# Performance work log

Hardware: AMD Instinct MI355X
Metric: run time of the kernel (lower is better)

The kernel has to match this reference:

```python
import jax, jax.numpy as jnp
import numpy as np

N, E, F, D, G, K = 50000, 1600000, 128, 256, 64, 10


def setup_inputs() -> dict:
    key = jax.random.key(0)
    ks = jax.random.split(key, 20)
    x = jax.random.normal(ks[0], (N, F), dtype=jnp.float32)
    edge_index = jax.random.randint(ks[1], (2, E), 0, N, dtype=jnp.int64)
    batch_index = jnp.sort(jax.random.randint(ks[2], (N,), 0, G, dtype=jnp.int64))

    def lin(k, fan_in, fan_out):
        w = jax.random.normal(k, (fan_in, fan_out), dtype=jnp.float32) / np.sqrt(fan_in)
        return w

    return {
        "x": x, "edge_index": edge_index, "batch_index": batch_index,
        "W0": lin(ks[3], F, D), "b0": jnp.zeros((D,), jnp.float32),
        "W1": lin(ks[4], D, D), "b1": jnp.zeros((D,), jnp.float32),
        "W2": lin(ks[5], D, D), "b2": jnp.zeros((D,), jnp.float32),
        "W3": lin(ks[6], D, D), "b3": jnp.zeros((D,), jnp.float32),
        "fc1_w": lin(ks[7], 2 * D, 512), "fc1_b": jnp.zeros((512,), jnp.float32),
        "fc2_w": lin(ks[8], 512, 256), "fc2_b": jnp.zeros((256,), jnp.float32),
        "out_w": lin(ks[9], 256, K), "out_b": jnp.zeros((K,), jnp.float32),
    }


def _gcn_conv(x, W, b, src, dst, dis):
    # PyG GCNConv: h = x W; out = D^{-1/2}(A+I)D^{-1/2} h + b  (self-loops added)
    h = x @ W                                   # [N, D]
    norm = dis[src] * dis[dst]                  # [E]
    msg = h[src] * norm[:, None]                # [E, D]
    agg = jax.ops.segment_sum(msg, dst, num_segments=x.shape[0])
    agg = agg + h * (dis * dis)[:, None]        # self-loop contribution
    return agg + b


def reference(x, edge_index, batch_index, W0, b0, W1, b1, W2, b2, W3, b3,
              fc1_w, fc1_b, fc2_w, fc2_b, out_w, out_b):
    src, dst = edge_index[0], edge_index[1]
    n = x.shape[0]
    # degree with self-loops
    deg = 1.0 + jax.ops.segment_sum(jnp.ones((src.shape[0],), jnp.float32), dst,
                                    num_segments=n)
    dis = jax.lax.rsqrt(deg)

    h = jnp.tanh(_gcn_conv(x, W0, b0, src, dst, dis))
    h = jnp.tanh(_gcn_conv(h, W1, b1, src, dst, dis))
    h = jnp.tanh(_gcn_conv(h, W2, b2, src, dst, dis))
    h = jnp.tanh(_gcn_conv(h, W3, b3, src, dst, dis))

    # global max pool + global mean pool over graphs in the batch
    gmax = jax.ops.segment_max(h, batch_index, num_segments=G)
    gsum = jax.ops.segment_sum(h, batch_index, num_segments=G)
    cnt = jax.ops.segment_sum(jnp.ones((n,), jnp.float32), batch_index,
                              num_segments=G)
    gmean = gsum / jnp.maximum(cnt, 1.0)[:, None]
    g = jnp.concatenate([gmax, gmean], axis=1)  # [G, 2D]

    g = jax.nn.relu(g @ fc1_w + fc1_b)
    g = jax.nn.relu(g @ fc2_w + fc2_b)
    return g @ out_w + out_b
```

## Files before the change

kernel.cpp:

```cpp
#include <hip/hip_runtime.h>
#include <hip/hip_bf16.h>


#define NNODES 50000
#define DDIM 256
#define SCAN_B 256
#define SCAN_G ((NNODES + SCAN_B - 1) / SCAN_B)

typedef __attribute__((ext_vector_type(8))) short short8;
typedef __attribute__((ext_vector_type(4))) float float4_;
typedef __attribute__((ext_vector_type(2))) float float2_;

__device__ __forceinline__ float fast_tanh(float x) {
    float e = __expf(2.0f * x);
    return 1.0f - 2.0f / (e + 1.0f);
}

__device__ __forceinline__ float bf2f(unsigned short u) {
    return __uint_as_float(((unsigned)u) << 16);
}
__device__ __forceinline__ unsigned short f2bf(float f) {
    unsigned u = __float_as_uint(f);
    u = u + 0x7fffu + ((u >> 16) & 1u);
    return (unsigned short)(u >> 16);
}

__device__ __forceinline__ unsigned f2key(float f) {
    unsigned b = __float_as_uint(f);
    return (b & 0x80000000u) ? ~b : (b | 0x80000000u);
}
__device__ __forceinline__ float key2f(unsigned k) {
    unsigned b = (k & 0x80000000u) ? (k & 0x7fffffffu) : ~k;
    return __uint_as_float(b);
}

__global__ void hist_kernel(const int* __restrict__ ei, int* __restrict__ deg,
                            int* __restrict__ rank, int E) {
    int e = blockIdx.x * blockDim.x + threadIdx.x;
    if (e < E) rank[e] = atomicAdd(&deg[ei[E + e]], 1);
}

__global__ void scan1_kernel(const int* __restrict__ deg, int* __restrict__ bsum, int N) {
    __shared__ int s[SCAN_B];
    int t = threadIdx.x;
    int idx = blockIdx.x * SCAN_B + t;
    s[t] = (idx < N) ? deg[idx] : 0;
    __syncthreads();
    for (int off = SCAN_B / 2; off > 0; off >>= 1) {
        if (t < off) s[t] += s[t + off];
        __syncthreads();
    }
    if (t == 0) bsum[blockIdx.x] = s[0];
}

__global__ void scan2_kernel(const int* __restrict__ deg, const int* __restrict__ bsum,
                             int* __restrict__ rowptr, float* __restrict__ dis, int N) {
    __shared__ int s[SCAN_B];
    __shared__ int bs[SCAN_B];
    int t = threadIdx.x;
    int bid = blockIdx.x;
    int idx = bid * SCAN_B + t;
    int d = (idx < N) ? deg[idx] : 0;
    s[t] = d;
    bs[t] = (t < bid) ? bsum[t] : 0;
    __syncthreads();
    for (int off = 1; off < SCAN_B; off <<= 1) {
        int v = (t >= off) ? s[t - off] : 0;
        __syncthreads();
        s[t] += v;
        __syncthreads();
    }
    for (int off = SCAN_B / 2; off > 0; off >>= 1) {
        if (t < off) bs[t] += bs[t + off];
        __syncthreads();
    }
    if (idx < N) {
        rowptr[idx] = bs[0] + s[t] - d;
        dis[idx] = rsqrtf(1.0f + (float)d);
    }
}

__global__ void scatter_kernel(const int* __restrict__ ei, const int* __restrict__ rowptr,
                               const int* __restrict__ rank, int* __restrict__ col, int E) {
    int e = blockIdx.x * blockDim.x + threadIdx.x;
    if (e < E) {
        int d = ei[E + e];
        col[rowptr[d] + rank[e]] = ei[e];
    }
}

__global__ void cast_x_kernel(const float* __restrict__ x, const float* __restrict__ dis,
                              unsigned short* __restrict__ xh, int total) {
    int i = blockIdx.x * blockDim.x + threadIdx.x;
    if (i < total) xh[i] = f2bf(x[i] * dis[i >> 7]);
}

__global__ void transpose_all_kernel(const float* __restrict__ W0, const float* __restrict__ W1,
                                     const float* __restrict__ W2, const float* __restrict__ W3,
                                     unsigned short* __restrict__ wt0, unsigned short* __restrict__ wt1,
                                     unsigned short* __restrict__ wt2, unsigned short* __restrict__ wt3) {
    int b = blockIdx.x;
    int n = threadIdx.x;
    const float* W; unsigned short* Wt; int K; int k;
    if (b < 128)      { W = W0; Wt = wt0; K = 128; k = b; }
    else if (b < 384) { W = W1; Wt = wt1; K = 256; k = b - 128; }
    else if (b < 640) { W = W2; Wt = wt2; K = 256; k = b - 384; }
    else              { W = W3; Wt = wt3; K = 256; k = b - 640; }
    Wt[n * K + k] = f2bf(W[k * 256 + n]);
}

__device__ __forceinline__ void paddu(float2_* acc, uint4 u) {
    float2_ v0 = {__uint_as_float(u.x << 16), __uint_as_float(u.x & 0xffff0000u)};
    float2_ v1 = {__uint_as_float(u.y << 16), __uint_as_float(u.y & 0xffff0000u)};
    float2_ v2 = {__uint_as_float(u.z << 16), __uint_as_float(u.z & 0xffff0000u)};
    float2_ v3 = {__uint_as_float(u.w << 16), __uint_as_float(u.w & 0xffff0000u)};
    acc[0] += v0; acc[1] += v1; acc[2] += v2; acc[3] += v3;
}
__device__ __forceinline__ void paddw(float2_* acc, uint4 u, float w) {
    float2_ w2 = {w, w};
    float2_ v0 = {__uint_as_float(u.x << 16), __uint_as_float(u.x & 0xffff0000u)};
    float2_ v1 = {__uint_as_float(u.y << 16), __uint_as_float(u.y & 0xffff0000u)};
    float2_ v2 = {__uint_as_float(u.z << 16), __uint_as_float(u.z & 0xffff0000u)};
    float2_ v3 = {__uint_as_float(u.w << 16), __uint_as_float(u.w & 0xffff0000u)};
    acc[0] += v0 * w2; acc[1] += v1 * w2; acc[2] += v2 * w2; acc[3] += v3 * w2;
}

template <int D, bool FINALIZE>
__global__ void msgpass_bf16(const unsigned short* __restrict__ in,
                             unsigned short* __restrict__ out,
                             const int* __restrict__ rowptr, const int* __restrict__ deg,
                             const int* __restrict__ col,
                             const float* __restrict__ dis, const float* __restrict__ bias) {
    constexpr int L = D / 8;
    constexpr int P = 64 / L;
    int lane = threadIdx.x & 63;
    int wav  = threadIdx.x >> 6;
    int n = blockIdx.x * 8 + wav;
    if (n >= NNODES) return;
    int part = lane / L;
    int sl   = lane % L;
    int start = rowptr[n];
    int cnt   = deg[n];
    float dn = dis[n];
    float2_ acc[4];
#pragma unroll
    for (int j = 0; j < 4; ++j) { float2_ z = {0.0f, 0.0f}; acc[j] = z; }

    int e = 0;
    for (; e + 4 * P <= cnt; e += 4 * P) {
        int c0 = col[start + e + part];
        int c1 = col[start + e + P + part];
        int c2 = col[start + e + 2 * P + part];
        int c3 = col[start + e + 3 * P + part];
        uint4 u0 = *((const uint4*)(in + (size_t)c0 * D) + sl);
        uint4 u1 = *((const uint4*)(in + (size_t)c1 * D) + sl);
        uint4 u2 = *((const uint4*)(in + (size_t)c2 * D) + sl);
        uint4 u3 = *((const uint4*)(in + (size_t)c3 * D) + sl);
        paddu(acc, u0);
        paddu(acc, u1);
        paddu(acc, u2);
        paddu(acc, u3);
    }
    for (; e + P <= cnt; e += P) {
        int c = col[start + e + part];
        uint4 u = *((const uint4*)(in + (size_t)c * D) + sl);
        paddu(acc, u);
    }
    int r = cnt - e;
    if (r > 0) {
        int c = (part < r) ? col[start + e + part] : n;
        float w = (part < r) ? 1.0f : 0.0f;
        uint4 u = *((const uint4*)(in + (size_t)c * D) + sl);
        paddw(acc, u, w);
    }
    {
        float w = (part == 0) ? 1.0f : 0.0f;
        uint4 u = *((const uint4*)(in + (size_t)n * D) + sl);
        paddw(acc, u, w);
    }
#pragma unroll
    for (int j = 0; j < 4; ++j) {
#pragma unroll
        for (int h = 0; h < 2; ++h) {
            if (P == 4) acc[j][h] += __shfl(acc[j][h], lane ^ 16);
            acc[j][h] += __shfl(acc[j][h], lane ^ 32);
        }
    }
    if (part == 0) {
        float a[8] = {acc[0][0], acc[0][1], acc[1][0], acc[1][1],
                      acc[2][0], acc[2][1], acc[3][0], acc[3][1]};
        if (FINALIZE) {
#pragma unroll
            for (int j = 0; j < 8; ++j)
                a[j] = fast_tanh(fmaf(a[j], dn, bias[sl * 8 + j]));
        } else {
#pragma unroll
            for (int j = 0; j < 8; ++j)
                a[j] *= dn;
        }
        uint4 o;
        o.x = (unsigned)f2bf(a[0]) | ((unsigned)f2bf(a[1]) << 16);
        o.y = (unsigned)f2bf(a[2]) | ((unsigned)f2bf(a[3]) << 16);
        o.z = (unsigned)f2bf(a[4]) | ((unsigned)f2bf(a[5]) << 16);
        o.w = (unsigned)f2bf(a[6]) | ((unsigned)f2bf(a[7]) << 16);
        *((uint4*)(out + (size_t)n * D) + sl) = o;
    }
}

template <int K, bool TANH>
__launch_bounds__(256, 2)
__global__ void gemm_mfma(const short* __restrict__ A, const short* __restrict__ Bt,
                          const float* __restrict__ bias, const float* __restrict__ dis,
                          unsigned short* __restrict__ C, int N) {
    constexpr int PK = 40;
    __shared__ __align__(16) short As[128 * PK];
    __shared__ __align__(16) short Bs[128 * PK];
    int t = threadIdx.x;
    int lane = t & 63;
    int w    = t >> 6;
    int wr = w & 1;
    int wc = w >> 1;
    int m0 = blockIdx.x * 128;
    int n0 = blockIdx.y * 128;

    int srow = t >> 2;
    int koff = (t & 3) * 8;
    int arow0 = m0 + srow;      if (arow0 > N - 1) arow0 = N - 1;
    int arow1 = m0 + 64 + srow; if (arow1 > N - 1) arow1 = N - 1;
    const short8* ap0 = (const short8*)(A + (size_t)arow0 * K + koff);
    const short8* ap1 = (const short8*)(A + (size_t)arow1 * K + koff);
    const short8* bp0 = (const short8*)(Bt + (size_t)(n0 + srow) * K + koff);
    const short8* bp1 = (const short8*)(Bt + (size_t)(n0 + 64 + srow) * K + koff);

    float4_ acc[4][4];
#pragma unroll
    for (int i = 0; i < 4; ++i)
#pragma unroll
        for (int j = 0; j < 4; ++j) {
            float4_ z = {0.0f, 0.0f, 0.0f, 0.0f};
            acc[i][j] = z;
        }

    short8 a0 = ap0[0], a1 = ap1[0], b0 = bp0[0], b1 = bp1[0];
    constexpr int NKB = K / 32;
    int g = lane >> 4;
    int r = lane & 15;

    for (int kb = 0; kb < NKB; ++kb) {
        __syncthreads();
        *(short8*)&As[srow * PK + koff]        = a0;
        *(short8*)&As[(64 + srow) * PK + koff] = a1;
        *(short8*)&Bs[srow * PK + koff]        = b0;
        *(short8*)&Bs[(64 + srow) * PK + koff] = b1;
        __syncthreads();
        if (kb + 1 < NKB) {
            a0 = ap0[(kb + 1) * 4];
            a1 = ap1[(kb + 1) * 4];
            b0 = bp0[(kb + 1) * 4];
            b1 = bp1[(kb + 1) * 4];
        }
        short8 af[4], bfr[4];
#pragma unroll
        for (int i = 0; i < 4; ++i)
            af[i] = *(const short8*)&As[(wr * 64 + i * 16 + r) * PK + g * 8];
#pragma unroll
        for (int j = 0; j < 4; ++j)
            bfr[j] = *(const short8*)&Bs[(wc * 64 + j * 16 + r) * PK + g * 8];
#pragma unroll
        for (int i = 0; i < 4; ++i)
#pragma unroll
            for (int j = 0; j < 4; ++j)
                acc[i][j] = __builtin_amdgcn_mfma_f32_16x16x32_bf16(af[i], bfr[j],
                                                                    acc[i][j], 0, 0, 0);
    }

#pragma unroll
    for (int i = 0; i < 4; ++i) {
        int rowb = m0 + wr * 64 + i * 16 + g * 4;
#pragma unroll
        for (int rr = 0; rr < 4; ++rr) {
            int row = rowb + rr;
            if (row < N) {
                float dsc = TANH ? 0.0f : dis[row];
#pragma unroll
                for (int j = 0; j < 4; ++j) {
                    int cb = n0 + wc * 64 + j * 16 + r;
                    float v = acc[i][j][rr];
                    if (TANH) v = fast_tanh(v + bias[cb]);
                    else      v = v * dsc;
                    C[(size_t)row * 256 + cb] = f2bf(v);
                }
            }
        }
    }
}

#define POOL_CHUNK 64
__global__ void pool_kernel(const unsigned short* __restrict__ act,
                            const int* __restrict__ batch,
                            float* __restrict__ gsum, unsigned* __restrict__ gmaxk,
                            int* __restrict__ gcnt, int N) {
    int t  = threadIdx.x;
    int n0 = blockIdx.x * POOL_CHUNK;
    if (n0 >= N) return;
    int n1 = n0 + POOL_CHUNK;
    if (n1 > N) n1 = N;
    int   cur = batch[n0];
    float sum = 0.0f, mx = -2.0f;
    int   run = 0;
    for (int n = n0; n < n1; ++n) {
        int g = batch[n];
        float v = bf2f(act[(size_t)n * DDIM + t]);
        if (g != cur) {
            atomicAdd(&gsum[cur * DDIM + t], sum);
            atomicMax(&gmaxk[cur * DDIM + t], f2key(mx));
            if (t == 0) atomicAdd(&gcnt[cur], run);
            cur = g; sum = 0.0f; mx = -2.0f; run = 0;
        }
        sum += v;
        mx = fmaxf(mx, v);
        run++;
    }
    atomicAdd(&gsum[cur * DDIM + t], sum);
    atomicMax(&gmaxk[cur * DDIM + t], f2key(mx));
    if (t == 0) atomicAdd(&gcnt[cur], run);
}

__global__ void mlp_kernel(const float* __restrict__ gsum, const unsigned* __restrict__ gmaxk,
                           const int* __restrict__ gcnt,
                           const float* __restrict__ fc1_w, const float* __restrict__ fc1_b,
                           const float* __restrict__ fc2_w, const float* __restrict__ fc2_b,
                           const float* __restrict__ out_w, const float* __restrict__ out_b,
                           float* __restrict__ out) {
    int g = blockIdx.x;
    int t = threadIdx.x;
    __shared__ float gv[512];
    __shared__ float t1[512];
    __shared__ float t2[256];
    float cnt = fmaxf((float)gcnt[g], 1.0f);
    gv[t]       = key2f(gmaxk[g * DDIM + t]);
    gv[256 + t] = gsum[g * DDIM + t] / cnt;
    __syncthreads();
    float a0 = fc1_b[t], a1 = fc1_b[t + 256];
    for (int k = 0; k < 512; ++k) {
        float gk = gv[k];
        a0 = fmaf(gk, fc1_w[k * 512 + t], a0);
        a1 = fmaf(gk, fc1_w[k * 512 + t + 256], a1);
    }
    t1[t]       = fmaxf(a0, 0.0f);
    t1[t + 256] = fmaxf(a1, 0.0f);
    __syncthreads();
    float b0 = fc2_b[t];
    for (int k = 0; k < 512; ++k)
        b0 = fmaf(t1[k], fc2_w[k * 256 + t], b0);
    t2[t] = fmaxf(b0, 0.0f);
    __syncthreads();
    if (t < 10) {
        float o = out_b[t];
        for (int k = 0; k < 256; ++k)
            o = fmaf(t2[k], out_w[k * 10 + t], o);
        out[g * 10 + t] = o;
    }
}

extern "C" void kernel_launch(void* const* d_in, const int* in_sizes, int n_in,
                              void* d_out, int out_size, void* d_ws, size_t ws_size,
                              hipStream_t stream) {
    const float* x      = (const float*)d_in[0];
    const int*   ei     = (const int*)d_in[1];
    const int*   batch  = (const int*)d_in[2];
    const float* W0     = (const float*)d_in[3];
    const float* b0     = (const float*)d_in[4];
    const float* W1     = (const float*)d_in[5];
    const float* b1     = (const float*)d_in[6];
    const float* W2     = (const float*)d_in[7];
    const float* b2     = (const float*)d_in[8];
    const float* W3     = (const float*)d_in[9];
    const float* b3     = (const float*)d_in[10];
    const float* fc1_w  = (const float*)d_in[11];
    const float* fc1_b  = (const float*)d_in[12];
    const float* fc2_w  = (const float*)d_in[13];
    const float* fc2_b  = (const float*)d_in[14];
    const float* out_w  = (const float*)d_in[15];
    const float* out_b  = (const float*)d_in[16];
    float* out = (float*)d_out;

    const int N = in_sizes[2];
    const int E = in_sizes[1] / 2;

    char* ws = (char*)d_ws;
    const size_t off_deg    = 0;
    const size_t off_gsum   = 200192;
    const size_t off_gmaxk  = 265728;
    const size_t off_gcnt   = 331264;
    const size_t ZERO_BYTES = 331776;
    const size_t off_dis    = 331776;
    const size_t off_rowptr = 531968;
    const size_t off_bsum   = 732160;
    const size_t off_col    = 932352;
    const size_t off_xh     = 7332352;
    const size_t off_wt0    = 20132352;
    const size_t off_wt1    = 20197888;
    const size_t off_wt2    = 20328960;
    const size_t off_wt3    = 20460032;
    const size_t off_bufA   = 20591104;
    const size_t off_bufB   = 46191104;

    int*            deg    = (int*)(ws + off_deg);
    float*          gsum   = (float*)(ws + off_gsum);
    unsigned*       gmaxk  = (unsigned*)(ws + off_gmaxk);
    int*            gcnt   = (int*)(ws + off_gcnt);
    float*          dis    = (float*)(ws + off_dis);
    int*            rowptr = (int*)(ws + off_rowptr);
    int*            bsum   = (int*)(ws + off_bsum);
    int*            col    = (int*)(ws + off_col);
    unsigned short* xh     = (unsigned short*)(ws + off_xh);
    short*          wt0    = (short*)(ws + off_wt0);
    short*          wt1    = (short*)(ws + off_wt1);
    short*          wt2    = (short*)(ws + off_wt2);
    short*          wt3    = (short*)(ws + off_wt3);
    unsigned short* bufA   = (unsigned short*)(ws + off_bufA);
    unsigned short* bufB   = (unsigned short*)(ws + off_bufB);
    int*            rank   = (int*)(ws + off_bufA);

    hipMemsetAsync(ws, 0, ZERO_BYTES, stream);

    hist_kernel<<<(E + 255) / 256, 256, 0, stream>>>(ei, deg, rank, E);
    scan1_kernel<<<SCAN_G, SCAN_B, 0, stream>>>(deg, bsum, N);
    scan2_kernel<<<SCAN_G, SCAN_B, 0, stream>>>(deg, bsum, rowptr, dis, N);
    scatter_kernel<<<(E + 255) / 256, 256, 0, stream>>>(ei, rowptr, rank, col, E);

    cast_x_kernel<<<(N * 128 + 255) / 256, 256, 0, stream>>>(x, dis, xh, N * 128);
    transpose_all_kernel<<<896, 256, 0, stream>>>(W0, W1, W2, W3,
                                                  (unsigned short*)wt0, (unsigned short*)wt1,
                                                  (unsigned short*)wt2, (unsigned short*)wt3);

    msgpass_bf16<128, false><<<(N + 7) / 8, 512, 0, stream>>>(
        xh, bufB, rowptr, deg, col, dis, nullptr);
    gemm_mfma<128, true><<<dim3((N + 127) / 128, 2), 256, 0, stream>>>(
        (const short*)bufB, wt0, b0, dis, bufA, N);

    const short* wts[3] = {wt1, wt2, wt3};
    const float* bs_[3] = {b1, b2, b3};
    for (int l = 0; l < 3; ++l) {
        gemm_mfma<256, false><<<dim3((N + 127) / 128, 2), 256, 0, stream>>>(
            (const short*)bufA, wts[l], nullptr, dis, bufB, N);
        msgpass_bf16<256, true><<<(N + 7) / 8, 512, 0, stream>>>(
            bufB, bufA, rowptr, deg, col, dis, bs_[l]);
    }

    pool_kernel<<<(N + POOL_CHUNK - 1) / POOL_CHUNK, 256, 0, stream>>>(
        bufA, batch, gsum, gmaxk, gcnt, N);
    mlp_kernel<<<64, 256, 0, stream>>>(gsum, gmaxk, gcnt, fc1_w, fc1_b, fc2_w, fc2_b,
                                       out_w, out_b, out);
}
```

Measured before the change: 720.8 us.

## Compress CSR column indices to 16-bit, fuse prep kernels, deepen GEMM K-tile

Column indices are stored as unsigned short, which halves CSR index traffic, and they are read with nontemporal loads in message passing. The x-cast and weight-transpose kernels are merged into one launch. The MFMA GEMM now stages 64-wide K tiles per sync, halving barrier count at the cost of more LDS. The 16-bit indices only hold because N=50000 fits below 65536, so this breaks for larger graphs.

```diff
diff --git a/kernel.cpp b/kernel.cpp
--- a/kernel.cpp
+++ b/kernel.cpp
@@ -81,32 +81,36 @@
 }
 
 __global__ void scatter_kernel(const int* __restrict__ ei, const int* __restrict__ rowptr,
-                               const int* __restrict__ rank, int* __restrict__ col, int E) {
+                               const int* __restrict__ rank,
+                               unsigned short* __restrict__ col, int E) {
     int e = blockIdx.x * blockDim.x + threadIdx.x;
     if (e < E) {
         int d = ei[E + e];
-        col[rowptr[d] + rank[e]] = ei[e];
-    }
-}
-
-__global__ void cast_x_kernel(const float* __restrict__ x, const float* __restrict__ dis,
-                              unsigned short* __restrict__ xh, int total) {
-    int i = blockIdx.x * blockDim.x + threadIdx.x;
-    if (i < total) xh[i] = f2bf(x[i] * dis[i >> 7]);
-}
-
-__global__ void transpose_all_kernel(const float* __restrict__ W0, const float* __restrict__ W1,
-                                     const float* __restrict__ W2, const float* __restrict__ W3,
-                                     unsigned short* __restrict__ wt0, unsigned short* __restrict__ wt1,
-                                     unsigned short* __restrict__ wt2, unsigned short* __restrict__ wt3) {
+        col[rowptr[d] + rank[e]] = (unsigned short)ei[e];
+    }
+}
+
+#define CAST_BLOCKS ((NNODES * 128) / 256)
+__global__ void prep_kernel(const float* __restrict__ x, const float* __restrict__ dis,
+                            unsigned short* __restrict__ xh,
+                            const float* __restrict__ W0, const float* __restrict__ W1,
+                            const float* __restrict__ W2, const float* __restrict__ W3,
+                            unsigned short* __restrict__ wt0, unsigned short* __restrict__ wt1,
+                            unsigned short* __restrict__ wt2, unsigned short* __restrict__ wt3) {
     int b = blockIdx.x;
-    int n = threadIdx.x;
+    int t = threadIdx.x;
+    if (b < CAST_BLOCKS) {
+        int i = b * 256 + t;
+        xh[i] = f2bf(x[i] * dis[i >> 7]);
+        return;
+    }
+    b -= CAST_BLOCKS;
     const float* W; unsigned short* Wt; int K; int k;
     if (b < 128)      { W = W0; Wt = wt0; K = 128; k = b; }
     else if (b < 384) { W = W1; Wt = wt1; K = 256; k = b - 128; }
     else if (b < 640) { W = W2; Wt = wt2; K = 256; k = b - 384; }
     else              { W = W3; Wt = wt3; K = 256; k = b - 640; }
-    Wt[n * K + k] = f2bf(W[k * 256 + n]);
+    Wt[t * K + k] = f2bf(W[k * 256 + t]);
 }
 
 __device__ __forceinline__ void paddu(float2_* acc, uint4 u) {
@@ -129,7 +133,7 @@
 __global__ void msgpass_bf16(const unsigned short* __restrict__ in,
                              unsigned short* __restrict__ out,
                              const int* __restrict__ rowptr, const int* __restrict__ deg,
-                             const int* __restrict__ col,
+                             const unsigned short* __restrict__ col,
                              const float* __restrict__ dis, const float* __restrict__ bias) {
     constexpr int L = D / 8;
     constexpr int P = 64 / L;
@@ -148,10 +152,10 @@
 
     int e = 0;
     for (; e + 4 * P <= cnt; e += 4 * P) {
-        int c0 = col[start + e + part];
-        int c1 = col[start + e + P + part];
-        int c2 = col[start + e + 2 * P + part];
-        int c3 = col[start + e + 3 * P + part];
+        int c0 = __builtin_nontemporal_load(&col[start + e + part]);
+        int c1 = __builtin_nontemporal_load(&col[start + e + P + part]);
+        int c2 = __builtin_nontemporal_load(&col[start + e + 2 * P + part]);
+        int c3 = __builtin_nontemporal_load(&col[start + e + 3 * P + part]);
         uint4 u0 = *((const uint4*)(in + (size_t)c0 * D) + sl);
         uint4 u1 = *((const uint4*)(in + (size_t)c1 * D) + sl);
         uint4 u2 = *((const uint4*)(in + (size_t)c2 * D) + sl);
@@ -162,13 +166,13 @@
         paddu(acc, u3);
     }
     for (; e + P <= cnt; e += P) {
-        int c = col[start + e + part];
+        int c = __builtin_nontemporal_load(&col[start + e + part]);
         uint4 u = *((const uint4*)(in + (size_t)c * D) + sl);
         paddu(acc, u);
     }
     int r = cnt - e;
     if (r > 0) {
-        int c = (part < r) ? col[start + e + part] : n;
+        int c = (part < r) ? (int)__builtin_nontemporal_load(&col[start + e + part]) : n;
         float w = (part < r) ? 1.0f : 0.0f;
         uint4 u = *((const uint4*)(in + (size_t)c * D) + sl);
         paddw(acc, u, w);
@@ -212,7 +216,7 @@
 __global__ void gemm_mfma(const short* __restrict__ A, const short* __restrict__ Bt,
                           const float* __restrict__ bias, const float* __restrict__ dis,
                           unsigned short* __restrict__ C, int N) {
-    constexpr int PK = 40;
+    constexpr int PK = 72;
     __shared__ __align__(16) short As[128 * PK];
     __shared__ __align__(16) short Bs[128 * PK];
     int t = threadIdx.x;
@@ -241,37 +245,49 @@
             acc[i][j] = z;
         }
 
-    short8 a0 = ap0[0], a1 = ap1[0], b0 = bp0[0], b1 = bp1[0];
-    constexpr int NKB = K / 32;
+    constexpr int NKB = K / 64;
     int g = lane >> 4;
     int r = lane & 15;
 
+    short8 a00 = ap0[0], a01 = ap0[4];
+    short8 a10 = ap1[0], a11 = ap1[4];
+    short8 b00 = bp0[0], b01 = bp0[4];
+    short8 b10 = bp1[0], b11 = bp1[4];
+
     for (int kb = 0; kb < NKB; ++kb) {
         __syncthreads();
-        *(short8*)&As[srow * PK + koff]        = a0;
-        *(short8*)&As[(64 + srow) * PK + koff] = a1;
-        *(short8*)&Bs[srow * PK + koff]        = b0;
-        *(short8*)&Bs[(64 + srow) * PK + koff] = b1;
+        *(short8*)&As[srow * PK + koff]             = a00;
+        *(short8*)&As[srow * PK + koff + 32]        = a01;
+        *(short8*)&As[(64 + srow) * PK + koff]      = a10;
+        *(short8*)&As[(64 + srow) * PK + koff + 32] = a11;
+        *(short8*)&Bs[srow * PK + koff]             = b00;
+        *(short8*)&Bs[srow * PK + koff + 32]        = b01;
+        *(short8*)&Bs[(64 + srow) * PK + koff]      = b10;
+        *(short8*)&Bs[(64 + srow) * PK + koff + 32] = b11;
         __syncthreads();
         if (kb + 1 < NKB) {
-            a0 = ap0[(kb + 1) * 4];
-            a1 = ap1[(kb + 1) * 4];
-            b0 = bp0[(kb + 1) * 4];
-            b1 = bp1[(kb + 1) * 4];
-        }
-        short8 af[4], bfr[4];
-#pragma unroll
-        for (int i = 0; i < 4; ++i)
-            af[i] = *(const short8*)&As[(wr * 64 + i * 16 + r) * PK + g * 8];
-#pragma unroll
-        for (int j = 0; j < 4; ++j)
-            bfr[j] = *(const short8*)&Bs[(wc * 64 + j * 16 + r) * PK + g * 8];
-#pragma unroll
-        for (int i = 0; i < 4; ++i)
+            int o = (kb + 1) * 8;
+            a00 = ap0[o]; a01 = ap0[o + 4];
+            a10 = ap1[o]; a11 = ap1[o + 4];
+            b00 = bp0[o]; b01 = bp0[o + 4];
+            b10 = bp1[o]; b11 = bp1[o + 4];
+        }
+#pragma unroll
+        for (int s = 0; s < 2; ++s) {
+            short8 af[4], bfr[4];
+#pragma unroll
+            for (int i = 0; i < 4; ++i)
+                af[i] = *(const short8*)&As[(wr * 64 + i * 16 + r) * PK + s * 32 + g * 8];
 #pragma unroll
             for (int j = 0; j < 4; ++j)
-                acc[i][j] = __builtin_amdgcn_mfma_f32_16x16x32_bf16(af[i], bfr[j],
-                                                                    acc[i][j], 0, 0, 0);
+                bfr[j] = *(const short8*)&Bs[(wc * 64 + j * 16 + r) * PK + s * 32 + g * 8];
+#pragma unroll
+            for (int i = 0; i < 4; ++i)
+#pragma unroll
+                for (int j = 0; j < 4; ++j)
+                    acc[i][j] = __builtin_amdgcn_mfma_f32_16x16x32_bf16(af[i], bfr[j],
+                                                                        acc[i][j], 0, 0, 0);
+        }
     }
 
 #pragma unroll
@@ -413,7 +429,7 @@
     float*          dis    = (float*)(ws + off_dis);
     int*            rowptr = (int*)(ws + off_rowptr);
     int*            bsum   = (int*)(ws + off_bsum);
-    int*            col    = (int*)(ws + off_col);
+    unsigned short* col    = (unsigned short*)(ws + off_col);
     unsigned short* xh     = (unsigned short*)(ws + off_xh);
     short*          wt0    = (short*)(ws + off_wt0);
     short*          wt1    = (short*)(ws + off_wt1);
@@ -430,10 +446,10 @@
     scan2_kernel<<<SCAN_G, SCAN_B, 0, stream>>>(deg, bsum, rowptr, dis, N);
     scatter_kernel<<<(E + 255) / 256, 256, 0, stream>>>(ei, rowptr, rank, col, E);
 
-    cast_x_kernel<<<(N * 128 + 255) / 256, 256, 0, stream>>>(x, dis, xh, N * 128);
-    transpose_all_kernel<<<896, 256, 0, stream>>>(W0, W1, W2, W3,
-                                                  (unsigned short*)wt0, (unsigned short*)wt1,
-                                                  (unsigned short*)wt2, (unsigned short*)wt3);
+    prep_kernel<<<CAST_BLOCKS + 896, 256, 0, stream>>>(
+        x, dis, xh, W0, W1, W2, W3,
+        (unsigned short*)wt0, (unsigned short*)wt1,
+        (unsigned short*)wt2, (unsigned short*)wt3);
 
     msgpass_bf16<128, false><<<(N + 7) / 8, 512, 0, stream>>>(
         xh, bufB, rowptr, deg, col, dis, nullptr);
```

Result: no change. 724.9 us (+0.6%).
